# Optimization experiments

Hardware: AMD Instinct MI355X
Metric: run time of the kernel (lower is better)

## Reference

```python
import jax, jax.numpy as jnp
import numpy as np

B, S, D, H, HD, WIN = 2, 2048, 2048, 16, 128, 1024
EPS = 1e-06
SCALE = HD ** -0.5


def rotate_half(x):
    x1 = x[..., : x.shape[-1] // 2]
    x2 = x[..., x.shape[-1] // 2 :]
    return jnp.concatenate((-x2, x1), axis=-1)


def setup_inputs() -> dict:
    key = jax.random.key(0)
    ks = jax.random.split(key, 6)
    hidden_states = jax.random.normal(ks[0], (B, S, D), jnp.float32)
    # RoPE tables (HF-style: freqs duplicated across the two halves)
    pos = jnp.arange(S, dtype=jnp.float32)
    inv_freq = 1.0 / (10000.0 ** (jnp.arange(0, HD, 2, dtype=jnp.float32) / HD))
    freqs = pos[:, None] * inv_freq[None, :]            # [S, HD/2]
    emb = jnp.concatenate([freqs, freqs], axis=-1)      # [S, HD]
    cos = jnp.broadcast_to(jnp.cos(emb)[None], (B, S, HD)).astype(jnp.float32)
    sin = jnp.broadcast_to(jnp.sin(emb)[None], (B, S, HD)).astype(jnp.float32)
    std = 1.0 / np.sqrt(D)
    Wq = jax.random.normal(ks[1], (D, H * HD), jnp.float32) * std
    Wk = jax.random.normal(ks[2], (D, H * HD), jnp.float32) * std
    Wv = jax.random.normal(ks[3], (D, H * HD), jnp.float32) * std
    Wo = jax.random.normal(ks[4], (H * HD, D), jnp.float32) * (1.0 / np.sqrt(H * HD))
    q_scale = jnp.ones((HD,), jnp.float32)
    k_scale = jnp.ones((HD,), jnp.float32)
    return {"hidden_states": hidden_states, "cos": cos, "sin": sin,
            "Wq": Wq, "Wk": Wk, "Wv": Wv, "Wo": Wo,
            "q_scale": q_scale, "k_scale": k_scale}


def _rmsnorm(x, scale):
    var = jnp.mean(x * x, axis=-1, keepdims=True)
    return scale * (x * jax.lax.rsqrt(var + EPS))


def reference(hidden_states, cos, sin, Wq, Wk, Wv, Wo, q_scale, k_scale):
    b, s, _ = hidden_states.shape
    q = (hidden_states @ Wq).reshape(b, s, H, HD)
    k = (hidden_states @ Wk).reshape(b, s, H, HD)
    v = (hidden_states @ Wv).reshape(b, s, H, HD)
    q = _rmsnorm(q, q_scale)
    k = _rmsnorm(k, k_scale)
    # RoPE, unsqueeze_dim=2 (head axis)
    c = cos[:, :, None, :]
    sn = sin[:, :, None, :]
    q = q * c + rotate_half(q) * sn
    k = k * c + rotate_half(k) * sn
    scores = jnp.einsum("bqhd,bkhd->bhqk", q, k) * SCALE  # [B,H,S,S]
    i = jnp.arange(s)[:, None]
    j = jnp.arange(s)[None, :]
    mask = (j <= i) & (j >= i - WIN)  # causal + sliding window
    scores = jnp.where(mask[None, None], scores, jnp.finfo(scores.dtype).min)
    probs = jax.nn.softmax(scores, axis=-1)
    out = jnp.einsum("bhqk,bkhd->bqhd", probs, v).reshape(b, s, H * HD)
    return out @ Wo
```

## Files before the change

kernel.cpp:

```cpp
#include <hip/hip_runtime.h>

#define B_ 2
#define S_ 2048
#define D_ 2048
#define H_ 16
#define HD_ 128
#define WIN_ 1024
#define M_ (B_*S_)
#define N_ (H_*HD_)
#define SCALE_ 0.08838834764831845f
#define CSHIFT_ 11.5f

typedef unsigned short u16;
typedef __attribute__((ext_vector_type(8))) short short8;
typedef __attribute__((ext_vector_type(4))) float f32x4;

__device__ __forceinline__ float b2f(u16 u) {
    union { unsigned int i; float f; } x; x.i = ((unsigned int)u) << 16; return x.f;
}
__device__ __forceinline__ u16 f2b(float f) {
    union { float f; unsigned int i; } x; x.f = f;
    unsigned int u = x.i;
    return (u16)((u + 0x7fffu + ((u >> 16) & 1u)) >> 16);
}

__device__ __forceinline__ void async_ld16(const u16* g, u16* l) {
    __builtin_amdgcn_global_load_lds(
        (const __attribute__((address_space(1))) unsigned int*)g,
        (__attribute__((address_space(3))) unsigned int*)l, 16, 0, 0);
}

__global__ __launch_bounds__(256) void prep_kernel(const float* __restrict__ hs, u16* __restrict__ hsb,
                                                   const float* __restrict__ W0, const float* __restrict__ W1,
                                                   const float* __restrict__ W2, const float* __restrict__ W3,
                                                   u16* __restrict__ O0, u16* __restrict__ O1,
                                                   u16* __restrict__ O2, u16* __restrict__ O3) {
    if (blockIdx.z == 4) {
        const int linear = blockIdx.y * 64 + blockIdx.x;
        int i = linear * 256 + threadIdx.x;
#pragma unroll
        for (int rep = 0; rep < 2; ++rep, i += 1048576) {
            float4 v = ((const float4*)hs)[i];
            ushort4 o;
            o.x = f2b(v.x); o.y = f2b(v.y); o.z = f2b(v.z); o.w = f2b(v.w);
            ((ushort4*)hsb)[i] = o;
        }
        return;
    }
    __shared__ float tile[32][33];
    const float* in; u16* out;
    switch (blockIdx.z) {
        case 0: in = W0; out = O0; break;
        case 1: in = W1; out = O1; break;
        case 2: in = W2; out = O2; break;
        default: in = W3; out = O3; break;
    }
    const int C = 2048, R = 2048;
    int c0 = blockIdx.x * 32, r0 = blockIdx.y * 32;
    int tx = threadIdx.x & 31, ty = threadIdx.x >> 5;
#pragma unroll
    for (int rr = ty; rr < 32; rr += 8)
        tile[rr][tx] = in[(long)(r0 + rr) * C + c0 + tx];
    __syncthreads();
#pragma unroll
    for (int cc = ty; cc < 32; cc += 8)
        out[(long)(c0 + cc) * R + r0 + tx] = f2b(tile[tx][cc]);
}

__global__ __launch_bounds__(256) void gemm_qkv_kernel(const u16* __restrict__ A,
                                                       const u16* __restrict__ Bt3,
                                                       u16* __restrict__ Qb,
                                                       u16* __restrict__ Kb,
                                                       u16* __restrict__ Vtb) {
    constexpr int Kk = 2048;
    __shared__ u16 As[128 * 32];
    __shared__ u16 Bs[128 * 32];

    const int tid  = threadIdx.x;
    const int m0   = blockIdx.y * 128, n0 = blockIdx.x * 128;
    const int wid  = tid >> 6, lane = tid & 63;
    const int wm   = (wid >> 1) * 64, wn = (wid & 1) * 64;
    const int quad = lane >> 4, lrow = lane & 15;
    const int lr4  = lane >> 2, lc4 = lane & 3;
    const int swz  = (lr4 >> 1) & 3;
    const int rsw  = (lrow >> 1) & 3;

    f32x4 acc[4][4];
#pragma unroll
    for (int a = 0; a < 4; ++a)
#pragma unroll
        for (int b = 0; b < 4; ++b) acc[a][b] = (f32x4)0.0f;

    for (int k0 = 0; k0 < Kk; k0 += 32) {
        __syncthreads();
#pragma unroll
        for (int it = 0; it < 2; ++it) {
            const int ra = (wid + 4 * it) * 16;
            async_ld16(&A  [(long)(m0 + ra + lr4) * Kk + k0 + ((lc4 ^ swz) * 8)], &As[ra * 32]);
            async_ld16(&Bt3[(long)(n0 + ra + lr4) * Kk + k0 + ((lc4 ^ swz) * 8)], &Bs[ra * 32]);
        }
        __syncthreads();

        short8 af[4], bf[4];
#pragma unroll
        for (int t = 0; t < 4; ++t)
            af[t] = *(const short8*)&As[(wm + t * 16 + lrow) * 32 + ((quad ^ rsw) * 8)];
#pragma unroll
        for (int t = 0; t < 4; ++t)
            bf[t] = *(const short8*)&Bs[(wn + t * 16 + lrow) * 32 + ((quad ^ rsw) * 8)];
#pragma unroll
        for (int tm = 0; tm < 4; ++tm)
#pragma unroll
            for (int tn = 0; tn < 4; ++tn)
                acc[tm][tn] = __builtin_amdgcn_mfma_f32_16x16x32_bf16(
                    af[tm], bf[tn], acc[tm][tn], 0, 0, 0);
    }

    const int seg = n0 >> 11;
#pragma unroll
    for (int tm = 0; tm < 4; ++tm)
#pragma unroll
        for (int tn = 0; tn < 4; ++tn) {
            const int colg = (n0 & 2047) + wn + tn * 16 + lrow;
            const int rowb = m0 + wm + tm * 16 + quad * 4;
            if (seg == 2) {
                const int b = rowb >> 11, s = rowb & (S_ - 1);
                const int h = colg >> 7, d = colg & (HD_ - 1);
                ushort4 pk;
                pk.x = f2b(acc[tm][tn][0]); pk.y = f2b(acc[tm][tn][1]);
                pk.z = f2b(acc[tm][tn][2]); pk.w = f2b(acc[tm][tn][3]);
                *(ushort4*)&Vtb[((long)((b * H_ + h) * HD_ + d)) * S_ + s] = pk;
            } else {
                u16* dst = (seg == 0) ? Qb : Kb;
#pragma unroll
                for (int r = 0; r < 4; ++r)
                    dst[(long)(rowb + r) * N_ + colg] = f2b(acc[tm][tn][r]);
            }
        }
}

__global__ __launch_bounds__(256) void gemm_out_kernel(const u16* __restrict__ A,
                                                       const u16* __restrict__ Bt,
                                                       float* __restrict__ C) {
    constexpr int Kk = 2048, Nn = 2048;
    __shared__ u16 As[128 * 32];
    __shared__ u16 Bs[128 * 32];

    const int tid  = threadIdx.x;
    const int m0   = blockIdx.y * 128, n0 = blockIdx.x * 128;
    const int wid  = tid >> 6, lane = tid & 63;
    const int wm   = (wid >> 1) * 64, wn = (wid & 1) * 64;
    const int quad = lane >> 4, lrow = lane & 15;
    const int lr4  = lane >> 2, lc4 = lane & 3;
    const int swz  = (lr4 >> 1) & 3;
    const int rsw  = (lrow >> 1) & 3;

    f32x4 acc[4][4];
#pragma unroll
    for (int a = 0; a < 4; ++a)
#pragma unroll
        for (int b = 0; b < 4; ++b) acc[a][b] = (f32x4)0.0f;

    for (int k0 = 0; k0 < Kk; k0 += 32) {
        __syncthreads();
#pragma unroll
        for (int it = 0; it < 2; ++it) {
            const int ra = (wid + 4 * it) * 16;
            async_ld16(&A [(long)(m0 + ra + lr4) * Kk + k0 + ((lc4 ^ swz) * 8)], &As[ra * 32]);
            async_ld16(&Bt[(long)(n0 + ra + lr4) * Kk + k0 + ((lc4 ^ swz) * 8)], &Bs[ra * 32]);
        }
        __syncthreads();

        short8 af[4], bf[4];
#pragma unroll
        for (int t = 0; t < 4; ++t)
            af[t] = *(const short8*)&As[(wm + t * 16 + lrow) * 32 + ((quad ^ rsw) * 8)];
#pragma unroll
        for (int t = 0; t < 4; ++t)
            bf[t] = *(const short8*)&Bs[(wn + t * 16 + lrow) * 32 + ((quad ^ rsw) * 8)];
#pragma unroll
        for (int tm = 0; tm < 4; ++tm)
#pragma unroll
            for (int tn = 0; tn < 4; ++tn)
                acc[tm][tn] = __builtin_amdgcn_mfma_f32_16x16x32_bf16(
                    af[tm], bf[tn], acc[tm][tn], 0, 0, 0);
    }

#pragma unroll
    for (int tm = 0; tm < 4; ++tm)
#pragma unroll
        for (int tn = 0; tn < 4; ++tn) {
            const int col  = n0 + wn + tn * 16 + lrow;
            const int rowb = m0 + wm + tm * 16 + quad * 4;
#pragma unroll
            for (int r = 0; r < 4; ++r)
                C[(long)(rowb + r) * Nn + col] = acc[tm][tn][r];
        }
}

__global__ __launch_bounds__(256) void norm_rope_kernel(u16* __restrict__ Q, u16* __restrict__ Kb,
                                                        const float* __restrict__ qsc,
                                                        const float* __restrict__ ksc,
                                                        const float* __restrict__ cosp,
                                                        const float* __restrict__ sinp) {
    u16* X = blockIdx.y ? Kb : Q;
    const float* scale = blockIdx.y ? ksc : qsc;
    int wid = threadIdx.x >> 6, lane = threadIdx.x & 63;
    int row = blockIdx.x * 4 + wid;
    int bs  = row >> 4;
    long off = (long)row * HD_;
    float x1 = b2f(X[off + lane]);
    float x2 = b2f(X[off + lane + 64]);
    float ss = x1 * x1 + x2 * x2;
#pragma unroll
    for (int o = 1; o < 64; o <<= 1) ss += __shfl_xor(ss, o);
    float inv = rsqrtf(ss * (1.0f / HD_) + 1e-6f);
    long cb = (long)(bs & (S_ - 1)) * HD_;
    float c1 = cosp[cb + lane],      s1 = sinp[cb + lane];
    float c2 = cosp[cb + lane + 64], s2 = sinp[cb + lane + 64];
    float n1 = scale[lane] * x1 * inv;
    float n2 = scale[lane + 64] * x2 * inv;
    X[off + lane]      = f2b(n1 * c1 - n2 * s1);
    X[off + lane + 64] = f2b(n2 * c2 + n1 * s2);
}

__global__ __launch_bounds__(256) void fattn_kernel(const u16* __restrict__ Q,
                                                    const u16* __restrict__ K,
                                                    const u16* __restrict__ Vt,
                                                    u16* __restrict__ O) {
    __shared__ u16 Ks[64 * 128];
    __shared__ u16 Vs[128 * 64];
    __shared__ u16 Ps[4][16 * 72];

    const int tid  = threadIdx.x;
    const int wid  = tid >> 6, lane = tid & 63;
    const int quad = lane >> 4, lrow = lane & 15;
    const int qb = 31 - (blockIdx.x & 31);
    const int h  = (blockIdx.x >> 5) & (H_ - 1);
    const int b  = blockIdx.x >> 9;
    const int q0  = qb * 64;
    const int q0w = q0 + wid * 16;

    short8 qf[4];
    const long qrow = ((long)(b * S_ + q0w + lrow) * H_ + h) * HD_;
#pragma unroll
    for (int c = 0; c < 4; ++c)
        qf[c] = *(const short8*)&Q[qrow + c * 32 + quad * 8];

    float l_r[4] = {0.f, 0.f, 0.f, 0.f};
    f32x4 oacc[8];
#pragma unroll
    for (int t = 0; t < 8; ++t) oacc[t] = (f32x4)0.0f;

    const int ktlo = (q0 - WIN_ > 0) ? (q0 - WIN_) : 0;
    const long kgbase = ((long)b * S_ * H_ + h) * HD_;
    const long vgbase = ((long)(b * H_ + h) * HD_) * S_;
    const int lxor = lrow & 7;

    for (int kt0 = ktlo; kt0 < q0 + 64; kt0 += 64) {
        __syncthreads();
#pragma unroll
        for (int it = 0; it < 4; ++it) {
            const int rb = (wid * 4 + it) * 4;
            const int row = rb + (lane >> 4);
            const int cg = (lane & 15) ^ (row & 7);
            async_ld16(&K[kgbase + (long)(kt0 + row) * (H_ * HD_) + cg * 8], &Ks[rb * 128]);
        }
#pragma unroll
        for (int it = 0; it < 4; ++it) {
            const int db = (wid * 4 + it) * 8;
            const int d = db + (lane >> 3);
            const int cg = (lane & 7) ^ (d & 7);
            async_ld16(&Vt[vgbase + (long)d * S_ + kt0 + cg * 8], &Vs[db * 64]);
        }
        __syncthreads();

        const bool active = (kt0 <= q0w + 15) && (kt0 + 63 >= q0w - WIN_);
        if (active) {
            f32x4 cs[4];
#pragma unroll
            for (int t = 0; t < 4; ++t) {
                cs[t] = (f32x4)0.0f;
                const int krow = (t * 16 + lrow) * 128;
#pragma unroll
                for (int c = 0; c < 4; ++c) {
                    short8 kf = *(const short8*)&Ks[krow + (((c * 4 + quad) ^ lxor) * 8)];
                    cs[t] = __builtin_amdgcn_mfma_f32_16x16x32_bf16(qf[c], kf, cs[t], 0, 0, 0);
                }
            }

            const bool full = (kt0 + 63 <= q0w) && (kt0 >= q0w + 15 - WIN_);
            if (!full) {
#pragma unroll
                for (int t = 0; t < 4; ++t) {
                    const int jc = kt0 + t * 16 + lrow;
#pragma unroll
                    for (int r = 0; r < 4; ++r) {
                        const int i = q0w + quad * 4 + r;
                        if (jc > i || jc < i - WIN_) cs[t][r] = -1e30f;
                    }
                }
            }

#pragma unroll
            for (int t = 0; t < 4; ++t)
#pragma unroll
                for (int r = 0; r < 4; ++r) {
                    float p = __expf(fmaf(cs[t][r], SCALE_, -CSHIFT_));
                    l_r[r] += p;
                    Ps[wid][(quad * 4 + r) * 72 + t * 16 + lrow] = f2b(p);
                }

            short8 pf0 = *(const short8*)&Ps[wid][lrow * 72 + quad * 8];
            short8 pf1 = *(const short8*)&Ps[wid][lrow * 72 + 32 + quad * 8];
#pragma unroll
            for (int t = 0; t < 8; ++t) {
                const int vrow = (t * 16 + lrow) * 64;
                short8 vf0 = *(const short8*)&Vs[vrow + ((quad ^ lxor) * 8)];
                short8 vf1 = *(const short8*)&Vs[vrow + (((quad + 4) ^ lxor) * 8)];
                oacc[t] = __builtin_amdgcn_mfma_f32_16x16x32_bf16(pf0, vf0, oacc[t], 0, 0, 0);
                oacc[t] = __builtin_amdgcn_mfma_f32_16x16x32_bf16(pf1, vf1, oacc[t], 0, 0, 0);
            }
        }
    }

    float inv[4];
#pragma unroll
    for (int r = 0; r < 4; ++r) {
        float v = l_r[r];
#pragma unroll
        for (int o = 1; o < 16; o <<= 1) v += __shfl_xor(v, o);
        inv[r] = 1.0f / v;
    }

#pragma unroll
    for (int t = 0; t < 8; ++t) {
        const int d = t * 16 + lrow;
#pragma unroll
        for (int r = 0; r < 4; ++r) {
            const int q = q0w + quad * 4 + r;
            O[(long)(b * S_ + q) * N_ + h * HD_ + d] = f2b(oacc[t][r] * inv[r]);
        }
    }
}

extern "C" void kernel_launch(void* const* d_in, const int* in_sizes, int n_in,
                              void* d_out, int out_size, void* d_ws, size_t ws_size,
                              hipStream_t stream) {
    const float* hs   = (const float*)d_in[0];
    const float* cosp = (const float*)d_in[1];
    const float* sinp = (const float*)d_in[2];
    const float* Wq   = (const float*)d_in[3];
    const float* Wk   = (const float*)d_in[4];
    const float* Wv   = (const float*)d_in[5];
    const float* Wo   = (const float*)d_in[6];
    const float* qsc  = (const float*)d_in[7];
    const float* ksc  = (const float*)d_in[8];
    float* out = (float*)d_out;

    char* ws = (char*)d_ws;
    const size_t MD = (size_t)M_ * D_;
    const size_t WN = (size_t)D_ * N_;
    u16* hsb = (u16*)ws;
    u16* Wqt = (u16*)(ws + MD * 2);
    u16* Wkt = Wqt + WN;
    u16* Wvt = Wkt + WN;
    u16* Wot = Wvt + WN;
    u16* Qb  = Wot + WN;
    u16* Kb  = Qb + MD;
    u16* Vtb = Kb + MD;
    u16* Ab  = hsb;

    dim3 gp(64, 64, 5);
    prep_kernel<<<gp, 256, 0, stream>>>(hs, hsb, Wq, Wk, Wv, Wo, Wqt, Wkt, Wvt, Wot);

    dim3 gqkv(48, 32);
    gemm_qkv_kernel<<<gqkv, 256, 0, stream>>>(hsb, Wqt, Qb, Kb, Vtb);

    dim3 gn(B_ * S_ * H_ / 4, 2);
    norm_rope_kernel<<<gn, 256, 0, stream>>>(Qb, Kb, qsc, ksc, cosp, sinp);

    fattn_kernel<<<B_ * H_ * (S_ / 64), 256, 0, stream>>>(Qb, Kb, Vtb, Ab);

    dim3 gout(16, 32);
    gemm_out_kernel<<<gout, 256, 0, stream>>>(Ab, Wot, out);
}
```

Measured before the change: 425.1 us.

## Widen attention query tile to 128 rows and vectorize norm-rope kernel

The attention kernel now handles 128 query rows per block with 512 threads (8 waves), so each K/V tile loaded into shared memory is reused by twice as many waves. The block-to-(batch, head, query-block) mapping is changed to pair reversed and forward query-block orders across two passes, to balance causal work. The norm+RoPE kernel now reads packed bf16 pairs, does the rotate-half through a cross-lane shuffle, and processes two rows per wave. Risks are lower occupancy or more register pressure with 512-thread blocks, and more masked wasted work in the larger diagonal tiles.

```diff
diff --git a/kernel.cpp b/kernel.cpp
--- a/kernel.cpp
+++ b/kernel.cpp
@@ -205,40 +205,48 @@
                                                         const float* __restrict__ sinp) {
     u16* X = blockIdx.y ? Kb : Q;
     const float* scale = blockIdx.y ? ksc : qsc;
-    int wid = threadIdx.x >> 6, lane = threadIdx.x & 63;
-    int row = blockIdx.x * 4 + wid;
-    int bs  = row >> 4;
-    long off = (long)row * HD_;
-    float x1 = b2f(X[off + lane]);
-    float x2 = b2f(X[off + lane + 64]);
-    float ss = x1 * x1 + x2 * x2;
-#pragma unroll
-    for (int o = 1; o < 64; o <<= 1) ss += __shfl_xor(ss, o);
-    float inv = rsqrtf(ss * (1.0f / HD_) + 1e-6f);
-    long cb = (long)(bs & (S_ - 1)) * HD_;
-    float c1 = cosp[cb + lane],      s1 = sinp[cb + lane];
-    float c2 = cosp[cb + lane + 64], s2 = sinp[cb + lane + 64];
-    float n1 = scale[lane] * x1 * inv;
-    float n2 = scale[lane + 64] * x2 * inv;
-    X[off + lane]      = f2b(n1 * c1 - n2 * s1);
-    X[off + lane + 64] = f2b(n2 * c2 + n1 * s2);
-}
-
-__global__ __launch_bounds__(256) void fattn_kernel(const u16* __restrict__ Q,
-                                                    const u16* __restrict__ K,
-                                                    const u16* __restrict__ Vt,
-                                                    u16* __restrict__ O) {
+    const int wid = threadIdx.x >> 6, lane = threadIdx.x & 63;
+    const float2 sc2 = ((const float2*)scale)[lane];
+    const float sgn = (lane < 32) ? -1.0f : 1.0f;
+#pragma unroll
+    for (int rep = 0; rep < 2; ++rep) {
+        const int row = blockIdx.x * 8 + rep * 4 + wid;
+        const int s   = (row >> 4) & (S_ - 1);
+        unsigned int v = ((const unsigned int*)X)[(long)row * 64 + lane];
+        float x0 = b2f((u16)(v & 0xffff)), x1 = b2f((u16)(v >> 16));
+        float ss = x0 * x0 + x1 * x1;
+#pragma unroll
+        for (int o = 1; o < 64; o <<= 1) ss += __shfl_xor(ss, o);
+        const float inv = rsqrtf(ss * (1.0f / HD_) + 1e-6f);
+        const float n0 = x0 * sc2.x * inv, n1 = x1 * sc2.y * inv;
+        const float p0 = __shfl_xor(n0, 32), p1 = __shfl_xor(n1, 32);
+        const float2 c2 = ((const float2*)(cosp + (long)s * HD_))[lane];
+        const float2 s2 = ((const float2*)(sinp + (long)s * HD_))[lane];
+        const float o0 = n0 * c2.x + sgn * p0 * s2.x;
+        const float o1 = n1 * c2.y + sgn * p1 * s2.y;
+        ((unsigned int*)X)[(long)row * 64 + lane] =
+            ((unsigned int)f2b(o1) << 16) | (unsigned int)f2b(o0);
+    }
+}
+
+__global__ __launch_bounds__(512, 4) void fattn_kernel(const u16* __restrict__ Q,
+                                                       const u16* __restrict__ K,
+                                                       const u16* __restrict__ Vt,
+                                                       u16* __restrict__ O) {
     __shared__ u16 Ks[64 * 128];
     __shared__ u16 Vs[128 * 64];
-    __shared__ u16 Ps[4][16 * 72];
+    __shared__ u16 Ps[8][16 * 72];
 
     const int tid  = threadIdx.x;
     const int wid  = tid >> 6, lane = tid & 63;
     const int quad = lane >> 4, lrow = lane & 15;
-    const int qb = 31 - (blockIdx.x & 31);
-    const int h  = (blockIdx.x >> 5) & (H_ - 1);
-    const int b  = blockIdx.x >> 9;
-    const int q0  = qb * 64;
+    const int i    = blockIdx.x & 15;
+    const int pass = blockIdx.x >> 8;
+    const int bh   = pass * 16 + ((blockIdx.x >> 4) & 15);
+    const int qb   = pass ? i : 15 - i;
+    const int h  = bh & (H_ - 1);
+    const int b  = bh >> 4;
+    const int q0  = qb * 128;
     const int q0w = q0 + wid * 16;
 
     short8 qf[4];
@@ -257,18 +265,18 @@
     const long vgbase = ((long)(b * H_ + h) * HD_) * S_;
     const int lxor = lrow & 7;
 
-    for (int kt0 = ktlo; kt0 < q0 + 64; kt0 += 64) {
-        __syncthreads();
-#pragma unroll
-        for (int it = 0; it < 4; ++it) {
-            const int rb = (wid * 4 + it) * 4;
+    for (int kt0 = ktlo; kt0 < q0 + 128; kt0 += 64) {
+        __syncthreads();
+#pragma unroll
+        for (int it = 0; it < 2; ++it) {
+            const int rb = (wid * 2 + it) * 4;
             const int row = rb + (lane >> 4);
             const int cg = (lane & 15) ^ (row & 7);
             async_ld16(&K[kgbase + (long)(kt0 + row) * (H_ * HD_) + cg * 8], &Ks[rb * 128]);
         }
 #pragma unroll
-        for (int it = 0; it < 4; ++it) {
-            const int db = (wid * 4 + it) * 8;
+        for (int it = 0; it < 2; ++it) {
+            const int db = (wid * 2 + it) * 8;
             const int d = db + (lane >> 3);
             const int cg = (lane & 7) ^ (d & 7);
             async_ld16(&Vt[vgbase + (long)d * S_ + kt0 + cg * 8], &Vs[db * 64]);
@@ -296,8 +304,8 @@
                     const int jc = kt0 + t * 16 + lrow;
 #pragma unroll
                     for (int r = 0; r < 4; ++r) {
-                        const int i = q0w + quad * 4 + r;
-                        if (jc > i || jc < i - WIN_) cs[t][r] = -1e30f;
+                        const int qi = q0w + quad * 4 + r;
+                        if (jc > qi || jc < qi - WIN_) cs[t][r] = -1e30f;
                     }
                 }
             }
@@ -377,10 +385,10 @@
     dim3 gqkv(48, 32);
     gemm_qkv_kernel<<<gqkv, 256, 0, stream>>>(hsb, Wqt, Qb, Kb, Vtb);
 
-    dim3 gn(B_ * S_ * H_ / 4, 2);
+    dim3 gn(B_ * S_ * H_ / 8, 2);
     norm_rope_kernel<<<gn, 256, 0, stream>>>(Qb, Kb, qsc, ksc, cosp, sinp);
 
-    fattn_kernel<<<B_ * H_ * (S_ / 64), 256, 0, stream>>>(Qb, Kb, Vtb, Ab);
+    fattn_kernel<<<B_ * H_ * (S_ / 128), 512, 0, stream>>>(Qb, Kb, Vtb, Ab);
 
     dim3 gout(16, 32);
     gemm_out_kernel<<<gout, 256, 0, stream>>>(Ab, Wot, out);
```

After: 390.9 us. 1.09x faster.
